# Optimization experiments

Hardware: AMD Instinct MI355X
Metric: run time of the kernel (lower is better)

The kernel has to match this reference:

```python
import jax, jax.numpy as jnp
import numpy as np

N_NODES = 50000
N_EDGES = 800000
D = 64
N_LAYERS = 3  # zip(convs(4), batchnorms(3)) truncates to 3 executed layers
N_GRAPHS = 32
EPS_BN = 1e-5
NEG_SLOPE = 0.2


def segment_softmax(logits, seg, n):
    m = jax.ops.segment_max(logits, seg, num_segments=n)
    m = jnp.where(jnp.isfinite(m), m, 0.0)
    z = jnp.exp(logits - m[seg])
    s = jax.ops.segment_sum(z, seg, num_segments=n)
    return z / (s[seg] + 1e-16)


def setup_inputs() -> dict:
    key = jax.random.key(0)
    ks = jax.random.split(key, 16)
    s = 0.1
    return {
        "x": jax.random.normal(ks[0], (N_NODES, D), jnp.float32),
        "edge_index": jax.random.randint(ks[1], (2, N_EDGES), 0, N_NODES),
        "edge_attr": jax.random.normal(ks[2], (N_EDGES, D), jnp.float32),
        "batch": jnp.sort(jax.random.randint(ks[3], (N_NODES,), 0, N_GRAPHS)),
        # EdgeConvLayer MLP params (stacked over layers)
        "em_w1": jax.random.normal(ks[4], (N_LAYERS, 3 * D, D)) * s,
        "em_b1": jnp.zeros((N_LAYERS, D)),
        "em_w2": jax.random.normal(ks[5], (N_LAYERS, D, D)) * s,
        "em_b2": jnp.zeros((N_LAYERS, D)),
        # GATConv params (heads=1, add_self_loops=False)
        "gat_w": jax.random.normal(ks[6], (N_LAYERS, D, D)) * s,
        "att_src": jax.random.normal(ks[7], (N_LAYERS, D)) * s,
        "att_dst": jax.random.normal(ks[8], (N_LAYERS, D)) * s,
        "edge_w": jax.random.normal(ks[9], (N_LAYERS, D, D)) * s,
        "att_edge": jax.random.normal(ks[10], (N_LAYERS, D)) * s,
        "gat_bias": jnp.zeros((N_LAYERS, D)),
        # BatchNorm params
        "bn_gamma": jnp.ones((N_LAYERS, D)),
        "bn_beta": jnp.zeros((N_LAYERS, D)),
        # readout MLP
        "mlp_w1": jax.random.normal(ks[11], (D, D)) * s,
        "mlp_b1": jnp.zeros((D,)),
        "mlp_w2": jax.random.normal(ks[12], (D, D // 2)) * s,
        "mlp_b2": jnp.zeros((D // 2,)),
        "mlp_w3": jax.random.normal(ks[13], (D // 2, 1)) * s,
        "mlp_b3": jnp.zeros((1,)),
    }


def reference(x, edge_index, edge_attr, batch, em_w1, em_b1, em_w2, em_b2,
              gat_w, att_src, att_dst, edge_w, att_edge, gat_bias,
              bn_gamma, bn_beta, mlp_w1, mlp_b1, mlp_w2, mlp_b2, mlp_w3, mlp_b3):
    row, col = edge_index[0], edge_index[1]
    n = x.shape[0]
    for l in range(N_LAYERS):
        # MetaLayer edge model: cat(src, dst, edge_attr) -> 2-layer MLP
        cat = jnp.concatenate([x[row], x[col], edge_attr], axis=1)  # (E, 3D)
        eh = jax.nn.relu(cat @ em_w1[l] + em_b1[l])
        edge_attr = eh @ em_w2[l] + em_b2[l]  # (E, D)
        # GATConv, heads=1: shared linear for src/dst
        xw = x @ gat_w[l]  # (N, D)
        a_edge = edge_attr @ (edge_w[l] @ att_edge[l])  # fused lin_edge + att_edge dot
        logits = (xw @ att_src[l])[row] + (xw @ att_dst[l])[col] + a_edge
        alpha = segment_softmax(jax.nn.leaky_relu(logits, NEG_SLOPE), col, n)
        h = jax.ops.segment_sum(alpha[:, None] * xw[row], col, num_segments=n) + gat_bias[l]
        # BatchNorm (training batch stats) + ReLU
        mu = h.mean(axis=0)
        var = h.var(axis=0)
        x = jax.nn.relu((h - mu) * jax.lax.rsqrt(var + EPS_BN) * bn_gamma[l] + bn_beta[l])
    # global mean pool over graphs
    sums = jax.ops.segment_sum(x, batch, num_segments=N_GRAPHS)
    cnt = jax.ops.segment_sum(jnp.ones((n,), x.dtype), batch, num_segments=N_GRAPHS)
    g = sums / jnp.maximum(cnt, 1.0)[:, None]
    h = jax.nn.relu(g @ mlp_w1 + mlp_b1)
    h = jax.nn.relu(h @ mlp_w2 + mlp_b2)
    return h @ mlp_w3 + mlp_b3  # (N_GRAPHS, 1)
```

## Files before the change

### kernel.cpp

```cpp
#include <hip/hip_runtime.h>


#define NN 50000
#define NE 800000
#define DP 68
#define NEG_SLOPE 0.2f

typedef __attribute__((ext_vector_type(8))) __bf16 bf16x8;
typedef __attribute__((ext_vector_type(4))) float f32x4;

__device__ __forceinline__ float4 ld4(const float* __restrict__ p){ return *(const float4* __restrict__)p; }
__device__ __forceinline__ void st4(float* __restrict__ p, float4 v){ *(float4* __restrict__)p = v; }
__device__ __forceinline__ float4 f4zero(){ return make_float4(0.f,0.f,0.f,0.f); }
__device__ __forceinline__ float4 f4add(float4 a, float4 b){
  return make_float4(a.x+b.x, a.y+b.y, a.z+b.z, a.w+b.w);
}
__device__ __forceinline__ float4 f4fma(float a, float4 b, float4 c){
  return make_float4(fmaf(a,b.x,c.x), fmaf(a,b.y,c.y), fmaf(a,b.z,c.z), fmaf(a,b.w,c.w));
}
__device__ __forceinline__ float f4dot(float4 a, float4 b){
  return fmaf(a.x,b.x, fmaf(a.y,b.y, fmaf(a.z,b.z, a.w*b.w)));
}
__device__ __forceinline__ bf16x8 cvt8(float4 a, float4 b){
  bf16x8 r;
  r[0]=(__bf16)a.x; r[1]=(__bf16)a.y; r[2]=(__bf16)a.z; r[3]=(__bf16)a.w;
  r[4]=(__bf16)b.x; r[5]=(__bf16)b.y; r[6]=(__bf16)b.z; r[7]=(__bf16)b.w;
  return r;
}
__device__ __forceinline__ bf16x8 addpack8(bf16x8 a, bf16x8 b){
  bf16x8 r;
#pragma unroll
  for (int e = 0; e < 8; ++e) r[e] = (__bf16)((float)a[e] + (float)b[e]);
  return r;
}
__device__ __forceinline__ ushort4 pack4(float4 v){
  ushort4 u;
  u.x = __builtin_bit_cast(unsigned short, (__bf16)v.x);
  u.y = __builtin_bit_cast(unsigned short, (__bf16)v.y);
  u.z = __builtin_bit_cast(unsigned short, (__bf16)v.z);
  u.w = __builtin_bit_cast(unsigned short, (__bf16)v.w);
  return u;
}
__device__ __forceinline__ float4 bnrelu4(float4 v, const float* sc, const float* sh, int d){
  return make_float4(
    fmaxf(fmaf(v.x, sc[d+0], sh[d+0]), 0.f),
    fmaxf(fmaf(v.y, sc[d+1], sh[d+1]), 0.f),
    fmaxf(fmaf(v.z, sc[d+2], sh[d+2]), 0.f),
    fmaxf(fmaf(v.w, sc[d+3], sh[d+3]), 0.f));
}

__device__ __forceinline__ void gemm_tile(const float* inT, const float* W,
                                          int el0, int d0, float4 acc[4]){
#pragma unroll 4
  for (int kc = 0; kc < 16; ++kc){
    float4 w0 = ld4(&W[(kc*4+0)*64 + d0]);
    float4 w1 = ld4(&W[(kc*4+1)*64 + d0]);
    float4 w2 = ld4(&W[(kc*4+2)*64 + d0]);
    float4 w3 = ld4(&W[(kc*4+3)*64 + d0]);
#pragma unroll
    for (int i = 0; i < 4; ++i){
      float4 iv = ld4(&inT[(el0+i)*DP + kc*4]);
      acc[i] = f4fma(iv.x, w0, acc[i]);
      acc[i] = f4fma(iv.y, w1, acc[i]);
      acc[i] = f4fma(iv.z, w2, acc[i]);
      acc[i] = f4fma(iv.w, w3, acc[i]);
    }
  }
}

__global__ __launch_bounds__(256) void setup_kernel(
    const int* __restrict__ ei_col, int* __restrict__ cnt,
    const int* __restrict__ batch, int* __restrict__ goff,
    const float* __restrict__ em_w1, const float* __restrict__ em_w2,
    const float* __restrict__ edge_w, const float* __restrict__ att_edge,
    __bf16* __restrict__ w1f, __bf16* __restrict__ w2f, float* __restrict__ vbuf)
{
  const int b = blockIdx.x, t = threadIdx.x;
  if (b < NE/256){
    atomicAdd(&cnt[ei_col[b*256 + t]], 1);
    int n = b*256 + t;
    if (n < NN){
      int bn = batch[n];
      int bp = (n == 0) ? -1 : batch[n-1];
      for (int g = bp + 1; g <= bn; ++g) goff[g] = n;
      if (n == NN - 1){ for (int g = bn + 1; g <= 32; ++g) goff[g] = NN; }
    }
  } else {
    const int l = b - NE/256;
    const float* W1 = em_w1 + l*12288 + 8192;
    const float* W2 = em_w2 + l*4096;
    for (int p = t; p < 512; p += 256){
      int li = p & 63, ks = (p >> 6) & 1, nt = p >> 7;
      int kbase = ks*32 + (li >> 4)*8;
      int j = nt*16 + (li & 15);
      bf16x8 v1, v2;
#pragma unroll
      for (int e = 0; e < 8; ++e){
        v1[e] = (__bf16)W1[(size_t)(kbase+e)*64 + j];
        v2[e] = (__bf16)W2[(size_t)(kbase+e)*64 + j];
      }
      *(bf16x8*)(w1f + (size_t)l*4096 + p*8) = v1;
      *(bf16x8*)(w2f + (size_t)l*4096 + p*8) = v2;
    }
    if (t < 64){
      float a = 0.f;
      const float* ew = edge_w + l*4096 + t*64;
      const float* ae = att_edge + l*64;
#pragma unroll 8
      for (int j = 0; j < 64; ++j) a = fmaf(ew[j], ae[j], a);
      vbuf[l*64 + t] = a;
    }
  }
}

__global__ __launch_bounds__(1024) void scan_kernel(const int* __restrict__ cnt,
                                                    int* __restrict__ off){
  __shared__ int wsum[16];
  __shared__ int carry_s;
  const int t = threadIdx.x;
  const int lane = t & 63, w = t >> 6;
  if (t == 0) carry_s = 0;
  __syncthreads();
  for (int base = 0; base < NN; base += 1024){
    int idx = base + t;
    int v = (idx < NN) ? cnt[idx] : 0;
    int x = v;
#pragma unroll
    for (int o = 1; o < 64; o <<= 1){
      int u = __shfl_up(x, o);
      if (lane >= o) x += u;
    }
    if (lane == 63) wsum[w] = x;
    __syncthreads();
    int wo = carry_s;
#pragma unroll
    for (int k = 0; k < 16; ++k) if (k < w) wo += wsum[k];
    int incl = x + wo;
    if (idx < NN) off[idx] = incl - v;
    __syncthreads();
    if (t == 1023) carry_s = incl;
    __syncthreads();
  }
  if (t == 0) off[NN] = carry_s;
}

__global__ __launch_bounds__(256) void scatter_kernel(
    const int* __restrict__ ei, const int* __restrict__ off, int* __restrict__ cur,
    int* __restrict__ srow, int* __restrict__ scol, int* __restrict__ perm){
  int e = blockIdx.x * 256 + threadIdx.x;
  int r = ei[e], c = ei[NE + e];
  int pos = off[c] + atomicAdd(&cur[c], 1);
  srow[pos] = r; scol[pos] = c; perm[pos] = e;
}

__global__ __launch_bounds__(256) void node_prep(
    const float* __restrict__ x0_in, const float* __restrict__ h_in,
    const float* __restrict__ bnpart,
    const float* __restrict__ gamma, const float* __restrict__ beta,
    const float* __restrict__ em_w1, const float* __restrict__ em_b1,
    const float* __restrict__ gat_w,
    const float* __restrict__ att_src, const float* __restrict__ att_dst,
    __bf16* __restrict__ xaH, __bf16* __restrict__ xbH, __bf16* __restrict__ xwH,
    float* __restrict__ ssrc, float* __restrict__ sdst, int l)
{
  __shared__ float xt[64*DP];
  __shared__ float Ws[64*64];
  __shared__ float asrc[64], adst[64], b1s[64];
  __shared__ float sc[64], sh[64];
  const int t = threadIdx.x;
  const int n0 = blockIdx.x * 64;
  const int p = blockIdx.y;

  if (l > 0){
    if (t < 64){
      float s = 0.f, s2 = 0.f;
#pragma unroll 8
      for (int k = 0; k < 64; ++k){
        s  += bnpart[k*128 + t];
        s2 += bnpart[k*128 + 64 + t];
      }
      float mu  = s * (1.0f / NN);
      float var = s2 * (1.0f / NN) - mu * mu;
      float iv  = rsqrtf(var + 1e-5f) * gamma[(l-1)*64 + t];
      sc[t] = iv;
      sh[t] = beta[(l-1)*64 + t] - mu * iv;
    }
    __syncthreads();
  }

  { int nl = t >> 2, q = t & 3;
    int n = n0 + nl;
    float4 v0, v1, v2, v3;
    if (n < NN){
      const float* src = ((l == 0) ? x0_in : h_in) + (size_t)n*64 + q*16;
      v0 = ld4(src); v1 = ld4(src+4); v2 = ld4(src+8); v3 = ld4(src+12);
      if (l > 0){
        v0 = bnrelu4(v0, sc, sh, q*16);
        v1 = bnrelu4(v1, sc, sh, q*16+4);
        v2 = bnrelu4(v2, sc, sh, q*16+8);
        v3 = bnrelu4(v3, sc, sh, q*16+12);
      }
    } else { v0 = v1 = v2 = v3 = f4zero(); }
    float* dst = &xt[nl*DP + q*16];
    st4(dst, v0); st4(dst+4, v1); st4(dst+8, v2); st4(dst+12, v3);
  }
  if (p == 2){
    if (t < 64) asrc[t] = att_src[l*64 + t];
    else if (t < 128) adst[t-64] = att_dst[l*64 + (t-64)];
  } else if (p == 0 && t < 64){
    b1s[t] = em_b1[l*64 + t];
  }
  const float* wp = (p == 0) ? (em_w1 + l*12288)
                  : (p == 1) ? (em_w1 + l*12288 + 4096)
                             : (gat_w + l*4096);
  for (int i = t; i < 1024; i += 256) st4(&Ws[i*4], ld4(wp + i*4));
  __syncthreads();

  const int nl0 = (t >> 4) << 2;
  const int d0  = (t & 15) << 2;
  __bf16* op = (p == 0) ? xaH : (p == 1) ? xbH : xwH;

  float4 acc[4] = {f4zero(), f4zero(), f4zero(), f4zero()};
  gemm_tile(xt, Ws, nl0, d0, acc);
  if (p == 0){
    float4 bb = ld4(&b1s[d0]);
#pragma unroll
    for (int i = 0; i < 4; ++i) acc[i] = f4add(acc[i], bb);
  }
#pragma unroll
  for (int i = 0; i < 4; ++i){
    int n = n0 + nl0 + i;
    if (n < NN) *(ushort4*)(op + (size_t)n*64 + d0) = pack4(acc[i]);
  }
  if (p == 2){
    float4 a4 = ld4(&asrc[d0]);
    float4 b4 = ld4(&adst[d0]);
    float ps[4], pd[4];
#pragma unroll
    for (int i = 0; i < 4; ++i){ ps[i] = f4dot(acc[i], a4); pd[i] = f4dot(acc[i], b4); }
#pragma unroll
    for (int off = 8; off; off >>= 1){
#pragma unroll
      for (int i = 0; i < 4; ++i){ ps[i] += __shfl_xor(ps[i], off); pd[i] += __shfl_xor(pd[i], off); }
    }
    if ((t & 15) == 0){
#pragma unroll
      for (int i = 0; i < 4; ++i){
        int n = n0 + nl0 + i;
        if (n < NN){ ssrc[n] = ps[i]; sdst[n] = pd[i]; }
      }
    }
  }
}

__global__ __launch_bounds__(256) void edge_mlp(
    const float* __restrict__ ea0,
    const __bf16* ea_in,
    __bf16* ea_out,
    const __bf16* __restrict__ xaH, const __bf16* __restrict__ xbH,
    const float* __restrict__ ssrc, const float* __restrict__ sdst,
    const int* __restrict__ srow, const int* __restrict__ scol,
    const int* __restrict__ permp,
    const __bf16* __restrict__ w1f, const __bf16* __restrict__ w2f,
    const float* __restrict__ b2v, const float* __restrict__ vv,
    float* __restrict__ lrelu, int store_ea)
{
  __shared__ __align__(16) __bf16 uvh[64*72];
  __shared__ __align__(16) unsigned ehw[2048];
  __shared__ float b2s[64], vs[64], sb[128];
  __shared__ int rs[128], cs[128], ps[128];
  const int t = threadIdx.x;
  const int w = t >> 6, l = t & 63, m = l & 15, kg = l >> 4;
  const int eb = blockIdx.x * 128;

  if (t < 128){ rs[t] = srow[eb+t]; cs[t] = scol[eb+t]; }
  else if (t < 192){ b2s[t-128] = b2v[t-128]; vs[t-128] = vv[t-128]; }
  if (permp && t < 128) ps[t] = permp[eb+t];
  __syncthreads();

  const bf16x8* B1 = (const bf16x8*)w1f;
  const bf16x8* B2 = (const bf16x8*)w2f;
  const f32x4 z4 = {0.f, 0.f, 0.f, 0.f};
  const int e_loc = t >> 2, q = t & 3;

  const int r0 = rs[e_loc],      c0 = cs[e_loc];
  const int r1 = rs[64 + e_loc], c1 = cs[64 + e_loc];
  const bf16x8* pa0 = (const bf16x8*)(xaH + (size_t)r0*64 + q*16);
  const bf16x8* pb0 = (const bf16x8*)(xbH + (size_t)c0*64 + q*16);
  const bf16x8* pa1 = (const bf16x8*)(xaH + (size_t)r1*64 + q*16);
  const bf16x8* pb1 = (const bf16x8*)(xbH + (size_t)c1*64 + q*16);
  bf16x8 g_a0l = pa0[0], g_a0h = pa0[1], g_b0l = pb0[0], g_b0h = pb0[1];
  bf16x8 g_a1l = pa1[0], g_a1h = pa1[1], g_b1l = pb1[0], g_b1h = pb1[1];
  float sb0 = 0.f, sb1 = 0.f;
  if (q == 0){ sb0 = ssrc[r0] + sdst[c0]; sb1 = ssrc[r1] + sdst[c1]; }

  bf16x8 A00, A01, A10, A11;
  { const int elA = 16*w + m;
    if (ea0){
      const float* s0 = ea0 + (size_t)ps[elA]*64 + kg*8;
      const float* s1 = ea0 + (size_t)ps[64+elA]*64 + kg*8;
      A00 = cvt8(ld4(s0),    ld4(s0+4));  A01 = cvt8(ld4(s0+32), ld4(s0+36));
      A10 = cvt8(ld4(s1),    ld4(s1+4));  A11 = cvt8(ld4(s1+32), ld4(s1+36));
    } else {
      const __bf16* s0 = ea_in + (size_t)(eb+elA)*64 + kg*8;
      const __bf16* s1 = ea_in + (size_t)(eb+64+elA)*64 + kg*8;
      A00 = *(const bf16x8*)s0;  A01 = *(const bf16x8*)(s0+32);
      A10 = *(const bf16x8*)s1;  A11 = *(const bf16x8*)(s1+32);
    }
  }

  *(bf16x8*)&uvh[e_loc*72 + q*16]     = addpack8(g_a0l, g_b0l);
  *(bf16x8*)&uvh[e_loc*72 + q*16 + 8] = addpack8(g_a0h, g_b0h);
  if (q == 0){ sb[e_loc] = sb0; sb[64 + e_loc] = sb1; }
  asm volatile("" ::: "memory");

  __bf16* esc = (__bf16*)ehw;
  auto tile_compute = [&](bf16x8 a0, bf16x8 a1, int tb){
    f32x4 acc[4];
#pragma unroll
    for (int nt = 0; nt < 4; ++nt){
      acc[nt] = __builtin_amdgcn_mfma_f32_16x16x32_bf16(a0, B1[(nt*2+0)*64 + l], z4, 0, 0, 0);
      acc[nt] = __builtin_amdgcn_mfma_f32_16x16x32_bf16(a1, B1[(nt*2+1)*64 + l], acc[nt], 0, 0, 0);
    }
#pragma unroll
    for (int nt = 0; nt < 4; ++nt){
      const int j = nt*16 + m;
#pragma unroll
      for (int r = 0; r < 4; ++r){
        const int erow = 16*w + 4*kg + r;
        float v = acc[nt][r] + (float)uvh[erow*72 + j];
        v = fmaxf(v, 0.f);
        const int piece = (w*2 + (nt>>1))*64 + (((nt&1)<<1) | (m>>3))*16 + 4*kg + r;
        esc[piece*8 + (m&7)] = (__bf16)v;
      }
    }
    asm volatile("" ::: "memory");
    bf16x8 a20 = *(const bf16x8*)(esc + (size_t)((w*2+0)*64 + kg*16 + m)*8);
    bf16x8 a21 = *(const bf16x8*)(esc + (size_t)((w*2+1)*64 + kg*16 + m)*8);
    f32x4 acc2[4];
#pragma unroll
    for (int nt = 0; nt < 4; ++nt){
      acc2[nt] = __builtin_amdgcn_mfma_f32_16x16x32_bf16(a20, B2[(nt*2+0)*64 + l], z4, 0, 0, 0);
      acc2[nt] = __builtin_amdgcn_mfma_f32_16x16x32_bf16(a21, B2[(nt*2+1)*64 + l], acc2[nt], 0, 0, 0);
    }
    float p0 = 0.f, p1 = 0.f, p2 = 0.f, p3 = 0.f;
#pragma unroll
    for (int nt = 0; nt < 4; ++nt){
      const int j = nt*16 + m;
      const float bj = b2s[j], vj = vs[j];
      float vr[4];
      vr[0] = acc2[nt][0] + bj; vr[1] = acc2[nt][1] + bj;
      vr[2] = acc2[nt][2] + bj; vr[3] = acc2[nt][3] + bj;
      if (store_ea){
        const size_t rowb = (size_t)(eb + tb + 16*w + 4*kg)*64 + (j & ~1);
#pragma unroll
        for (int r = 0; r < 4; ++r){
          unsigned short hu = __builtin_bit_cast(unsigned short, (__bf16)vr[r]);
          int pu = __shfl_xor((int)hu, 1);
          if (!(m & 1)){
            unsigned word = (unsigned)hu | ((unsigned)(pu & 0xffff) << 16);
            *(unsigned*)(ea_out + rowb + (size_t)r*64) = word;
          }
        }
      }
      p0 = fmaf(vr[0], vj, p0); p1 = fmaf(vr[1], vj, p1);
      p2 = fmaf(vr[2], vj, p2); p3 = fmaf(vr[3], vj, p3);
    }
#pragma unroll
    for (int o = 8; o; o >>= 1){
      p0 += __shfl_xor(p0, o); p1 += __shfl_xor(p1, o);
      p2 += __shfl_xor(p2, o); p3 += __shfl_xor(p3, o);
    }
    if (m == 0){
      float pv[4] = {p0, p1, p2, p3};
#pragma unroll
      for (int r = 0; r < 4; ++r){
        const int erow = 16*w + 4*kg + r;
        float logit = sb[tb + erow] + pv[r];
        lrelu[eb + tb + erow] = logit > 0.f ? logit : NEG_SLOPE * logit;
      }
    }
  };

  tile_compute(A00, A01, 0);
  asm volatile("" ::: "memory");
  *(bf16x8*)&uvh[e_loc*72 + q*16]     = addpack8(g_a1l, g_b1l);
  *(bf16x8*)&uvh[e_loc*72 + q*16 + 8] = addpack8(g_a1h, g_b1h);
  asm volatile("" ::: "memory");
  tile_compute(A10, A11, 64);
}

__global__ __launch_bounds__(256) void col_agg(
    const float* __restrict__ lrelu, const int* __restrict__ srow,
    const int* __restrict__ off, const __bf16* __restrict__ xwH,
    float* __restrict__ h)
{
  __shared__ float zS[4][128];
  __shared__ int   rS[4][128];
  const int t = threadIdx.x;
  const int lane = t & 63;
  const int wv = t >> 6;
  const int c = blockIdx.x * 4 + wv;
  const int s0 = off[c], s1 = off[c+1];
  const int L = s1 - s0;

  float l0 = (lane < L)    ? lrelu[s0+lane]    : -3.402823466e38f;
  float l1 = (lane+64 < L) ? lrelu[s0+64+lane] : -3.402823466e38f;
  int   r0 = (lane < L)    ? srow[s0+lane]     : 0;
  int   r1 = (lane+64 < L) ? srow[s0+64+lane]  : 0;

  float m = fmaxf(l0, l1);
  for (int i = lane+128; i < L; i += 64) m = fmaxf(m, lrelu[s0+i]);
#pragma unroll
  for (int o = 32; o; o >>= 1) m = fmaxf(m, __shfl_xor(m, o));

  float z0 = (lane < L)    ? expf(l0 - m) : 0.f;
  float z1 = (lane+64 < L) ? expf(l1 - m) : 0.f;
  float s = z0 + z1;
  for (int i = lane+128; i < L; i += 64) s += expf(lrelu[s0+i] - m);
#pragma unroll
  for (int o = 32; o; o >>= 1) s += __shfl_xor(s, o);
  const float inv = 1.f / (s + 1e-16f);

  zS[wv][lane] = z0;  zS[wv][64+lane] = z1;
  rS[wv][lane] = r0;  rS[wv][64+lane] = r1;
  asm volatile("" ::: "memory");

  float hv0 = 0.f, hv1 = 0.f, hv2 = 0.f, hv3 = 0.f;
  float hv4 = 0.f, hv5 = 0.f, hv6 = 0.f, hv7 = 0.f;
  if (L <= 128){
    int i = 0;
    for (; i + 8 <= L; i += 8){
      float za = zS[wv][i],   zb = zS[wv][i+1], zc = zS[wv][i+2], zd = zS[wv][i+3];
      float ze = zS[wv][i+4], zf = zS[wv][i+5], zg = zS[wv][i+6], zh = zS[wv][i+7];
      int   ra = rS[wv][i],   rb = rS[wv][i+1], rc = rS[wv][i+2], rd = rS[wv][i+3];
      int   re = rS[wv][i+4], rf = rS[wv][i+5], rg = rS[wv][i+6], rh = rS[wv][i+7];
      hv0 = fmaf(za, (float)xwH[(size_t)ra*64 + lane], hv0);
      hv1 = fmaf(zb, (float)xwH[(size_t)rb*64 + lane], hv1);
      hv2 = fmaf(zc, (float)xwH[(size_t)rc*64 + lane], hv2);
      hv3 = fmaf(zd, (float)xwH[(size_t)rd*64 + lane], hv3);
      hv4 = fmaf(ze, (float)xwH[(size_t)re*64 + lane], hv4);
      hv5 = fmaf(zf, (float)xwH[(size_t)rf*64 + lane], hv5);
      hv6 = fmaf(zg, (float)xwH[(size_t)rg*64 + lane], hv6);
      hv7 = fmaf(zh, (float)xwH[(size_t)rh*64 + lane], hv7);
    }
    for (; i < L; ++i)
      hv0 = fmaf(zS[wv][i], (float)xwH[(size_t)rS[wv][i]*64 + lane], hv0);
  } else {
    for (int i = 0; i < L; ++i){
      float z = expf(lrelu[s0+i] - m);
      int r = srow[s0+i];
      hv0 = fmaf(z, (float)xwH[(size_t)r*64 + lane], hv0);
    }
  }
  float hv = ((hv0 + hv1) + (hv2 + hv3)) + ((hv4 + hv5) + (hv6 + hv7));
  h[(size_t)c*64 + lane] = hv * inv;
}

__global__ __launch_bounds__(256) void bn_stats(
    const float* __restrict__ h, float* __restrict__ bnpart)
{
  const int g = blockIdx.x;
  const int t = threadIdx.x;
  const int d = t & 63, sub = t >> 6;
  const int n0 = g * 782;
  const int n1 = (n0 + 782 < NN) ? n0 + 782 : NN;
  float s = 0.f, s2 = 0.f;
  for (int n = n0 + sub; n < n1; n += 4){
    float v = h[(size_t)n*64 + d];
    s += v; s2 = fmaf(v, v, s2);
  }
  __shared__ float r1[4][64], r2[4][64];
  r1[sub][d] = s; r2[sub][d] = s2;
  __syncthreads();
  if (sub == 0){
    s  = r1[0][d] + r1[1][d] + r1[2][d] + r1[3][d];
    s2 = r2[0][d] + r2[1][d] + r2[2][d] + r2[3][d];
    bnpart[g*128 + d]      = s;
    bnpart[g*128 + 64 + d] = s2;
  }
}

__global__ __launch_bounds__(256) void seg_pool(
    const float* __restrict__ h, const int* __restrict__ goff,
    const float* __restrict__ bnpart,
    const float* __restrict__ gamma2, const float* __restrict__ beta2,
    float* __restrict__ pools, float* __restrict__ pcnt)
{
  __shared__ float sc[64], sh[64];
  const int g = blockIdx.x;
  const int t = threadIdx.x;
  const int d = t & 63, sub = t >> 6;
  if (t < 64){
    float s = 0.f, s2 = 0.f;
#pragma unroll 8
    for (int k = 0; k < 64; ++k){
      s  += bnpart[k*128 + t];
      s2 += bnpart[k*128 + 64 + t];
    }
    float mu  = s * (1.0f / NN);
    float var = s2 * (1.0f / NN) - mu * mu;
    float iv  = rsqrtf(var + 1e-5f) * gamma2[t];
    sc[t] = iv;
    sh[t] = beta2[t] - mu * iv;
  }
  __syncthreads();
  const int s0 = goff[g], s1 = goff[g+1];
  float s = 0.f;
  for (int n = s0 + sub; n < s1; n += 4)
    s += fmaxf(fmaf(h[(size_t)n*64 + d], sc[d], sh[d]), 0.f);
  __shared__ float r[4][64];
  r[sub][d] = s;
  __syncthreads();
  if (sub == 0){
    s = r[0][d] + r[1][d] + r[2][d] + r[3][d];
    pools[g*64 + d] = s;
    if (d == 0) pcnt[g] = (float)(s1 - s0);
  }
}

__global__ __launch_bounds__(256) void final_mlp(
    const float* __restrict__ pools, const float* __restrict__ pcnt,
    const float* __restrict__ w1, const float* __restrict__ b1,
    const float* __restrict__ w2, const float* __restrict__ b2,
    const float* __restrict__ w3, const float* __restrict__ b3,
    float* __restrict__ out)
{
  __shared__ float g[32*64], h1[32*64], h2[32*32];
  const int t = threadIdx.x;
  for (int i = t; i < 2048; i += 256) g[i] = pools[i] / fmaxf(pcnt[i >> 6], 1.0f);
  __syncthreads();
  for (int i = t; i < 2048; i += 256){
    int gi = i >> 6, d = i & 63;
    float a = b1[d];
    for (int k = 0; k < 64; ++k) a = fmaf(g[gi*64 + k], w1[k*64 + d], a);
    h1[i] = fmaxf(a, 0.f);
  }
  __syncthreads();
  for (int i = t; i < 1024; i += 256){
    int gi = i >> 5, d = i & 31;
    float a = b2[d];
    for (int k = 0; k < 64; ++k) a = fmaf(h1[gi*64 + k], w2[k*32 + d], a);
    h2[i] = fmaxf(a, 0.f);
  }
  __syncthreads();
  if (t < 32){
    float a = b3[0];
    for (int k = 0; k < 32; ++k) a = fmaf(h2[t*32 + k], w3[k], a);
    out[t] = a;
  }
}

extern "C" void kernel_launch(void* const* d_in, const int* in_sizes, int n_in,
                              void* d_out, int out_size, void* d_ws, size_t ws_size,
                              hipStream_t stream)
{
  (void)in_sizes; (void)n_in; (void)out_size; (void)ws_size;
  const float* x0       = (const float*)d_in[0];
  const int*   ei       = (const int*)  d_in[1];
  const float* ea0      = (const float*)d_in[2];
  const int*   batch    = (const int*)  d_in[3];
  const float* em_w1    = (const float*)d_in[4];
  const float* em_b1    = (const float*)d_in[5];
  const float* em_w2    = (const float*)d_in[6];
  const float* em_b2    = (const float*)d_in[7];
  const float* gat_w    = (const float*)d_in[8];
  const float* att_src  = (const float*)d_in[9];
  const float* att_dst  = (const float*)d_in[10];
  const float* edge_w   = (const float*)d_in[11];
  const float* att_edge = (const float*)d_in[12];
  const float* bn_gamma = (const float*)d_in[14];
  const float* bn_beta  = (const float*)d_in[15];
  const float* mlp_w1   = (const float*)d_in[16];
  const float* mlp_b1   = (const float*)d_in[17];
  const float* mlp_w2   = (const float*)d_in[18];
  const float* mlp_b2   = (const float*)d_in[19];
  const float* mlp_w3   = (const float*)d_in[20];
  const float* mlp_b3   = (const float*)d_in[21];
  float* out = (float*)d_out;

  const size_t N64 = (size_t)NN * 64, E64 = (size_t)NE * 64;
  float* ws    = (float*)d_ws;
  float* wsE   = ws;
  float* sxa   = wsE + E64;
  float* sxb   = sxa + N64;
  float* sxw   = sxb + N64;
  float* hbuf  = sxw + N64;
  float* bnpart= hbuf + N64;
  float* lrelu = bnpart + 64*128;
  float* pools = lrelu + NE;
  float* pcnt  = pools + 2048;
  float* ssrc  = pcnt + 32;
  float* sdst  = ssrc + NN;
  int*   cnt   = (int*)(sdst + NN);
  int*   cur   = cnt + NN;
  int*   soff  = cur + NN;
  int*   srow  = soff + NN + 1;
  int*   scol  = srow + NE;
  int*   perm  = scol + NE;
  int*   goff  = perm + NE;
  __bf16* eaB  = (__bf16*)wsE;
  __bf16* xaH  = (__bf16*)sxa;
  __bf16* xbH  = (__bf16*)sxb;
  __bf16* xwH  = (__bf16*)sxw;
  __bf16* w1f  = (__bf16*)(goff + 40);
  __bf16* w2f  = w1f + 3*4096;
  float* vbuf  = (float*)(w2f + 3*4096);

  hipMemsetAsync(cnt, 0, 2 * NN * sizeof(int), stream);
  setup_kernel<<<NE/256 + 3, 256, 0, stream>>>(
      ei + NE, cnt, batch, goff, em_w1, em_w2, edge_w, att_edge, w1f, w2f, vbuf);
  scan_kernel<<<1, 1024, 0, stream>>>(cnt, soff);
  scatter_kernel<<<NE / 256, 256, 0, stream>>>(ei, soff, cur, srow, scol, perm);

  for (int l = 0; l < 3; ++l){
    dim3 npg((NN + 63) / 64, 3);
    node_prep<<<npg, 256, 0, stream>>>(
        x0, hbuf, bnpart, bn_gamma, bn_beta,
        em_w1, em_b1, gat_w, att_src, att_dst, xaH, xbH, xwH, ssrc, sdst, l);

    edge_mlp<<<NE / 128, 256, 0, stream>>>(
        (l == 0) ? ea0 : nullptr, eaB, eaB, xaH, xbH, ssrc, sdst,
        srow, scol, (l == 0) ? perm : nullptr,
        w1f + (size_t)l*4096, w2f + (size_t)l*4096,
        em_b2 + l*64, vbuf + l*64, lrelu, (l < 2) ? 1 : 0);

    col_agg<<<NN / 4, 256, 0, stream>>>(lrelu, srow, soff, xwH, hbuf);

    bn_stats<<<64, 256, 0, stream>>>(hbuf, bnpart);
  }

  seg_pool<<<32, 256, 0, stream>>>(hbuf, goff, bnpart,
                                   bn_gamma + 128, bn_beta + 128, pools, pcnt);
  final_mlp<<<1, 256, 0, stream>>>(pools, pcnt, mlp_w1, mlp_b1, mlp_w2, mlp_b2,
                                   mlp_w3, mlp_b3, out);
}
```

Baseline: 823.3 us.

## Use bf16 MFMA for node_prep GEMMs and fuse the three projections per block

node_prep now computes the three node projections (edge-MLP src and dst halves plus the GAT linear) with bf16 MFMA instructions, replacing the scalar fp32 FMA tile. One block handles all three projections and stages the node features in LDS once, so the 3x grid.y launch and the repeated feature loads go away. The three weight matrices are pre-packed into MFMA fragment layout as bf16 in setup_kernel. Rounding inputs to bf16 before the GEMM adds error compared with the fp32 path, and the output is written as 32-bit pairs built with lane shuffles.

```diff
diff --git a/kernel.cpp b/kernel.cpp
--- a/kernel.cpp
+++ b/kernel.cpp
@@ -3,24 +3,13 @@
 
 #define NN 50000
 #define NE 800000
-#define DP 68
 #define NEG_SLOPE 0.2f
 
 typedef __attribute__((ext_vector_type(8))) __bf16 bf16x8;
 typedef __attribute__((ext_vector_type(4))) float f32x4;
 
 __device__ __forceinline__ float4 ld4(const float* __restrict__ p){ return *(const float4* __restrict__)p; }
-__device__ __forceinline__ void st4(float* __restrict__ p, float4 v){ *(float4* __restrict__)p = v; }
 __device__ __forceinline__ float4 f4zero(){ return make_float4(0.f,0.f,0.f,0.f); }
-__device__ __forceinline__ float4 f4add(float4 a, float4 b){
-  return make_float4(a.x+b.x, a.y+b.y, a.z+b.z, a.w+b.w);
-}
-__device__ __forceinline__ float4 f4fma(float a, float4 b, float4 c){
-  return make_float4(fmaf(a,b.x,c.x), fmaf(a,b.y,c.y), fmaf(a,b.z,c.z), fmaf(a,b.w,c.w));
-}
-__device__ __forceinline__ float f4dot(float4 a, float4 b){
-  return fmaf(a.x,b.x, fmaf(a.y,b.y, fmaf(a.z,b.z, a.w*b.w)));
-}
 __device__ __forceinline__ bf16x8 cvt8(float4 a, float4 b){
   bf16x8 r;
   r[0]=(__bf16)a.x; r[1]=(__bf16)a.y; r[2]=(__bf16)a.z; r[3]=(__bf16)a.w;
@@ -32,14 +21,6 @@
 #pragma unroll
   for (int e = 0; e < 8; ++e) r[e] = (__bf16)((float)a[e] + (float)b[e]);
   return r;
-}
-__device__ __forceinline__ ushort4 pack4(float4 v){
-  ushort4 u;
-  u.x = __builtin_bit_cast(unsigned short, (__bf16)v.x);
-  u.y = __builtin_bit_cast(unsigned short, (__bf16)v.y);
-  u.z = __builtin_bit_cast(unsigned short, (__bf16)v.z);
-  u.w = __builtin_bit_cast(unsigned short, (__bf16)v.w);
-  return u;
 }
 __device__ __forceinline__ float4 bnrelu4(float4 v, const float* sc, const float* sh, int d){
   return make_float4(
@@ -49,31 +30,14 @@
     fmaxf(fmaf(v.w, sc[d+3], sh[d+3]), 0.f));
 }
 
-__device__ __forceinline__ void gemm_tile(const float* inT, const float* W,
-                                          int el0, int d0, float4 acc[4]){
-#pragma unroll 4
-  for (int kc = 0; kc < 16; ++kc){
-    float4 w0 = ld4(&W[(kc*4+0)*64 + d0]);
-    float4 w1 = ld4(&W[(kc*4+1)*64 + d0]);
-    float4 w2 = ld4(&W[(kc*4+2)*64 + d0]);
-    float4 w3 = ld4(&W[(kc*4+3)*64 + d0]);
-#pragma unroll
-    for (int i = 0; i < 4; ++i){
-      float4 iv = ld4(&inT[(el0+i)*DP + kc*4]);
-      acc[i] = f4fma(iv.x, w0, acc[i]);
-      acc[i] = f4fma(iv.y, w1, acc[i]);
-      acc[i] = f4fma(iv.z, w2, acc[i]);
-      acc[i] = f4fma(iv.w, w3, acc[i]);
-    }
-  }
-}
-
 __global__ __launch_bounds__(256) void setup_kernel(
     const int* __restrict__ ei_col, int* __restrict__ cnt,
     const int* __restrict__ batch, int* __restrict__ goff,
     const float* __restrict__ em_w1, const float* __restrict__ em_w2,
+    const float* __restrict__ gat_w,
     const float* __restrict__ edge_w, const float* __restrict__ att_edge,
-    __bf16* __restrict__ w1f, __bf16* __restrict__ w2f, float* __restrict__ vbuf)
+    __bf16* __restrict__ w1f, __bf16* __restrict__ w2f, __bf16* __restrict__ wnf,
+    float* __restrict__ vbuf)
 {
   const int b = blockIdx.x, t = threadIdx.x;
   if (b < NE/256){
@@ -87,8 +51,8 @@
     }
   } else {
     const int l = b - NE/256;
-    const float* W1 = em_w1 + l*12288 + 8192;
-    const float* W2 = em_w2 + l*4096;
+    const float* W1c = em_w1 + l*12288 + 8192;
+    const float* W2  = em_w2 + l*4096;
     for (int p = t; p < 512; p += 256){
       int li = p & 63, ks = (p >> 6) & 1, nt = p >> 7;
       int kbase = ks*32 + (li >> 4)*8;
@@ -96,11 +60,24 @@
       bf16x8 v1, v2;
 #pragma unroll
       for (int e = 0; e < 8; ++e){
-        v1[e] = (__bf16)W1[(size_t)(kbase+e)*64 + j];
+        v1[e] = (__bf16)W1c[(size_t)(kbase+e)*64 + j];
         v2[e] = (__bf16)W2[(size_t)(kbase+e)*64 + j];
       }
       *(bf16x8*)(w1f + (size_t)l*4096 + p*8) = v1;
       *(bf16x8*)(w2f + (size_t)l*4096 + p*8) = v2;
+    }
+    for (int pp = t; pp < 1536; pp += 256){
+      int p = pp >> 9, piece = pp & 511;
+      int li = piece & 63, ks = (piece >> 6) & 1, nt = piece >> 7;
+      int kbase = ks*32 + (li >> 4)*8;
+      int j = nt*16 + (li & 15);
+      const float* W = (p == 0) ? (em_w1 + l*12288)
+                     : (p == 1) ? (em_w1 + l*12288 + 4096)
+                                : (gat_w + l*4096);
+      bf16x8 v;
+#pragma unroll
+      for (int e = 0; e < 8; ++e) v[e] = (__bf16)W[(size_t)(kbase+e)*64 + j];
+      *(bf16x8*)(wnf + (size_t)l*12288 + (size_t)p*4096 + piece*8) = v;
     }
     if (t < 64){
       float a = 0.f;
@@ -157,19 +134,18 @@
     const float* __restrict__ x0_in, const float* __restrict__ h_in,
     const float* __restrict__ bnpart,
     const float* __restrict__ gamma, const float* __restrict__ beta,
-    const float* __restrict__ em_w1, const float* __restrict__ em_b1,
-    const float* __restrict__ gat_w,
-    const float* __restrict__ att_src, const float* __restrict__ att_dst,
+    const __bf16* __restrict__ wnf_l,
+    const float* __restrict__ b1v,
+    const float* __restrict__ asrc_g, const float* __restrict__ adst_g,
     __bf16* __restrict__ xaH, __bf16* __restrict__ xbH, __bf16* __restrict__ xwH,
     float* __restrict__ ssrc, float* __restrict__ sdst, int l)
 {
-  __shared__ float xt[64*DP];
-  __shared__ float Ws[64*64];
-  __shared__ float asrc[64], adst[64], b1s[64];
+  __shared__ __align__(16) __bf16 xf[64*72];
   __shared__ float sc[64], sh[64];
+  __shared__ float b1s[64], asrc[64], adst[64];
   const int t = threadIdx.x;
   const int n0 = blockIdx.x * 64;
-  const int p = blockIdx.y;
+  const int w = t >> 6, lane = t & 63, m = lane & 15, kg = lane >> 4;
 
   if (l > 0){
     if (t < 64){
@@ -187,9 +163,13 @@
     }
     __syncthreads();
   }
-
-  { int nl = t >> 2, q = t & 3;
-    int n = n0 + nl;
+  if (t < 64) b1s[t] = b1v[t];
+  else if (t < 128) asrc[t-64] = asrc_g[t-64];
+  else if (t < 192) adst[t-128] = adst_g[t-128];
+
+  {
+    const int e_loc = t >> 2, q = t & 3;
+    const int n = n0 + e_loc;
     float4 v0, v1, v2, v3;
     if (n < NN){
       const float* src = ((l == 0) ? x0_in : h_in) + (size_t)n*64 + q*16;
@@ -201,53 +181,61 @@
         v3 = bnrelu4(v3, sc, sh, q*16+12);
       }
     } else { v0 = v1 = v2 = v3 = f4zero(); }
-    float* dst = &xt[nl*DP + q*16];
-    st4(dst, v0); st4(dst+4, v1); st4(dst+8, v2); st4(dst+12, v3);
-  }
-  if (p == 2){
-    if (t < 64) asrc[t] = att_src[l*64 + t];
-    else if (t < 128) adst[t-64] = att_dst[l*64 + (t-64)];
-  } else if (p == 0 && t < 64){
-    b1s[t] = em_b1[l*64 + t];
-  }
-  const float* wp = (p == 0) ? (em_w1 + l*12288)
-                  : (p == 1) ? (em_w1 + l*12288 + 4096)
-                             : (gat_w + l*4096);
-  for (int i = t; i < 1024; i += 256) st4(&Ws[i*4], ld4(wp + i*4));
-  __syncthreads();
-
-  const int nl0 = (t >> 4) << 2;
-  const int d0  = (t & 15) << 2;
-  __bf16* op = (p == 0) ? xaH : (p == 1) ? xbH : xwH;
-
-  float4 acc[4] = {f4zero(), f4zero(), f4zero(), f4zero()};
-  gemm_tile(xt, Ws, nl0, d0, acc);
-  if (p == 0){
-    float4 bb = ld4(&b1s[d0]);
-#pragma unroll
-    for (int i = 0; i < 4; ++i) acc[i] = f4add(acc[i], bb);
-  }
-#pragma unroll
-  for (int i = 0; i < 4; ++i){
-    int n = n0 + nl0 + i;
-    if (n < NN) *(ushort4*)(op + (size_t)n*64 + d0) = pack4(acc[i]);
-  }
-  if (p == 2){
-    float4 a4 = ld4(&asrc[d0]);
-    float4 b4 = ld4(&adst[d0]);
-    float ps[4], pd[4];
-#pragma unroll
-    for (int i = 0; i < 4; ++i){ ps[i] = f4dot(acc[i], a4); pd[i] = f4dot(acc[i], b4); }
-#pragma unroll
-    for (int off = 8; off; off >>= 1){
-#pragma unroll
-      for (int i = 0; i < 4; ++i){ ps[i] += __shfl_xor(ps[i], off); pd[i] += __shfl_xor(pd[i], off); }
-    }
-    if ((t & 15) == 0){
-#pragma unroll
-      for (int i = 0; i < 4; ++i){
-        int n = n0 + nl0 + i;
-        if (n < NN){ ssrc[n] = ps[i]; sdst[n] = pd[i]; }
+    *(bf16x8*)&xf[e_loc*72 + q*16]     = cvt8(v0, v1);
+    *(bf16x8*)&xf[e_loc*72 + q*16 + 8] = cvt8(v2, v3);
+  }
+  __syncthreads();
+
+  const bf16x8 a0 = *(const bf16x8*)&xf[(16*w + m)*72 + kg*8];
+  const bf16x8 a1 = *(const bf16x8*)&xf[(16*w + m)*72 + kg*8 + 32];
+  const f32x4 z4 = {0.f, 0.f, 0.f, 0.f};
+
+#pragma unroll
+  for (int p = 0; p < 3; ++p){
+    const bf16x8* Bp = (const bf16x8*)(wnf_l + (size_t)p*4096);
+    f32x4 acc[4];
+#pragma unroll
+    for (int nt = 0; nt < 4; ++nt){
+      acc[nt] = __builtin_amdgcn_mfma_f32_16x16x32_bf16(a0, Bp[(nt*2+0)*64 + lane], z4, 0, 0, 0);
+      acc[nt] = __builtin_amdgcn_mfma_f32_16x16x32_bf16(a1, Bp[(nt*2+1)*64 + lane], acc[nt], 0, 0, 0);
+    }
+    __bf16* op = (p == 0) ? xaH : (p == 1) ? xbH : xwH;
+#pragma unroll
+    for (int nt = 0; nt < 4; ++nt){
+      const int j = nt*16 + m;
+      const float bb = (p == 0) ? b1s[j] : 0.f;
+#pragma unroll
+      for (int r = 0; r < 4; ++r){
+        float v = acc[nt][r] + bb;
+        unsigned short hu = __builtin_bit_cast(unsigned short, (__bf16)v);
+        int pu = __shfl_xor((int)hu, 1);
+        if (!(m & 1)){
+          const int n = n0 + 16*w + 4*kg + r;
+          if (n < NN){
+            unsigned word = (unsigned)hu | ((unsigned)(pu & 0xffff) << 16);
+            *(unsigned*)(op + (size_t)n*64 + (j & ~1)) = word;
+          }
+        }
+      }
+    }
+    if (p == 2){
+#pragma unroll
+      for (int r = 0; r < 4; ++r){
+        float s1 = 0.f, s2 = 0.f;
+#pragma unroll
+        for (int nt = 0; nt < 4; ++nt){
+          s1 = fmaf(acc[nt][r], asrc[nt*16 + m], s1);
+          s2 = fmaf(acc[nt][r], adst[nt*16 + m], s2);
+        }
+#pragma unroll
+        for (int o = 8; o; o >>= 1){
+          s1 += __shfl_xor(s1, o);
+          s2 += __shfl_xor(s2, o);
+        }
+        if (m == 0){
+          const int n = n0 + 16*w + 4*kg + r;
+          if (n < NN){ ssrc[n] = s1; sdst[n] = s2; }
+        }
       }
     }
   }
@@ -605,19 +593,21 @@
   __bf16* xwH  = (__bf16*)sxw;
   __bf16* w1f  = (__bf16*)(goff + 40);
   __bf16* w2f  = w1f + 3*4096;
-  float* vbuf  = (float*)(w2f + 3*4096);
+  __bf16* wnf  = w2f + 3*4096;
+  float* vbuf  = (float*)(wnf + 3*12288);
 
   hipMemsetAsync(cnt, 0, 2 * NN * sizeof(int), stream);
   setup_kernel<<<NE/256 + 3, 256, 0, stream>>>(
-      ei + NE, cnt, batch, goff, em_w1, em_w2, edge_w, att_edge, w1f, w2f, vbuf);
+      ei + NE, cnt, batch, goff, em_w1, em_w2, gat_w, edge_w, att_edge,
+      w1f, w2f, wnf, vbuf);
   scan_kernel<<<1, 1024, 0, stream>>>(cnt, soff);
   scatter_kernel<<<NE / 256, 256, 0, stream>>>(ei, soff, cur, srow, scol, perm);
 
   for (int l = 0; l < 3; ++l){
-    dim3 npg((NN + 63) / 64, 3);
-    node_prep<<<npg, 256, 0, stream>>>(
+    node_prep<<<(NN + 63) / 64, 256, 0, stream>>>(
         x0, hbuf, bnpart, bn_gamma, bn_beta,
-        em_w1, em_b1, gat_w, att_src, att_dst, xaH, xbH, xwH, ssrc, sdst, l);
+        wnf + (size_t)l*12288, em_b1 + l*64, att_src + l*64, att_dst + l*64,
+        xaH, xbH, xwH, ssrc, sdst, l);
 
     edge_mlp<<<NE / 128, 256, 0, stream>>>(
         (l == 0) ? ea0 : nullptr, eaB, eaB, xaH, xbH, ssrc, sdst,
```

Result: faster. 788.0 us (-4.3%).
